# Optimization experiments

Measured on AMD Instinct MI355X. Metric: run time of the kernel, lower is better.

Reference implementation:

```python
import jax, jax.numpy as jnp
import numpy as np

B, L, D = 4, 896, 2048
HQ, HKV, HD = 32, 8, 64
GROUP = HQ // HKV          # 4
TOKENS_PER_FRAME = 7
ROPE_BASE = 10000.0


def setup_inputs() -> dict:
    key = jax.random.key(0)
    ks = jax.random.split(key, 5)
    s = 0.02
    return {
        "x": jax.random.normal(ks[0], (B, L, D), jnp.float32),
        "wq": jax.random.normal(ks[1], (D, D), jnp.float32) * s,
        "wk": jax.random.normal(ks[2], (D, HKV * HD), jnp.float32) * s,
        "wv": jax.random.normal(ks[3], (D, HKV * HD), jnp.float32) * s,
        "wo": jax.random.normal(ks[4], (D, D), jnp.float32) * s,
        "pos_ids": jnp.arange(L, dtype=jnp.int32),
    }


def _apply_rotary(t, cos, sin):
    # t: [B, L, H, HD]; rotate all HD dims, interleaved pairs.
    Bt, Lt, Ht, Hd = t.shape
    tp = t.reshape(Bt, Lt, Ht, Hd // 2, 2)
    x1, x2 = tp[..., 0], tp[..., 1]
    c = cos[None, :, None, :]   # [1, L, 1, HD/2]
    s = sin[None, :, None, :]
    y1 = x1 * c - x2 * s
    y2 = x1 * s + x2 * c
    return jnp.stack([y1, y2], axis=-1).reshape(Bt, Lt, Ht, Hd)


def reference(x, wq, wk, wv, wo, pos_ids):
    Bx, Lx, Dx = x.shape
    q = (x @ wq).reshape(Bx, Lx, HQ, HD)
    k = (x @ wk).reshape(Bx, Lx, HKV, HD)
    v = (x @ wv).reshape(Bx, Lx, HKV, HD)

    # RoPE (rot_dim = head_dim), scale = 1.0
    half = HD // 2
    inv_freq = 1.0 / (ROPE_BASE ** (jnp.arange(half, dtype=jnp.float32) / half))
    freqs = pos_ids.astype(jnp.float32)[:, None] * inv_freq[None, :]  # [L, HD/2]
    cos, sin = jnp.cos(freqs), jnp.sin(freqs)
    q = _apply_rotary(q, cos, sin)
    k = _apply_rotary(k, cos, sin)

    # GQA: expand kv heads to q heads (kv_head = q_head // GROUP)
    k = jnp.repeat(k, GROUP, axis=2)   # [B, L, HQ, HD]
    v = jnp.repeat(v, GROUP, axis=2)

    scale = 1.0 / jnp.sqrt(jnp.float32(HD))
    scores = jnp.einsum('blhd,bmhd->bhlm', q, k) * scale  # [B, HQ, L, L]

    # frame-block causal mask: allow key frame <= query frame
    pos = jnp.arange(Lx)
    fid = pos // TOKENS_PER_FRAME
    allow = fid[None, :] <= fid[:, None]                  # [L, L]
    neg = jnp.finfo(scores.dtype).min
    scores = jnp.where(allow[None, None], scores, neg)

    probs = jax.nn.softmax(scores, axis=-1)
    out = jnp.einsum('bhlm,bmhd->blhd', probs, v).reshape(Bx, Lx, Dx)
    return out @ wo
```

## Files before the change

kernel.cpp:

```cpp
#include <hip/hip_runtime.h>
#include <hip/hip_bf16.h>
#include <cstdint>

typedef __bf16 bf16;
typedef __bf16 bf16x8 __attribute__((ext_vector_type(8)));
typedef float floatx4 __attribute__((ext_vector_type(4)));

#define B_   4
#define L_   896
#define D_   2048
#define HQ_  32
#define HKV_ 8
#define HD_  64
#define NQKV 3072
#define M_   3584

__device__ inline void gl_lds16(const bf16* g, bf16* l) {
    __builtin_amdgcn_global_load_lds(
        (const __attribute__((address_space(1))) void*)g,
        (__attribute__((address_space(3))) void*)l, 16, 0, 0);
}

__device__ inline void barrier_() {
    asm volatile("" ::: "memory");
    __builtin_amdgcn_s_barrier();
    asm volatile("" ::: "memory");
}

__global__ __launch_bounds__(256) void convert_to_bf16(const float* __restrict__ in,
                                                       bf16* __restrict__ out) {
    long q = (long)blockIdx.x * 256 + threadIdx.x;
    float4 v = ((const float4*)in)[q];
    union { bf16 b[4]; ushort4 u; } w;
    w.b[0] = (bf16)v.x; w.b[1] = (bf16)v.y; w.b[2] = (bf16)v.z; w.b[3] = (bf16)v.w;
    ((ushort4*)out)[q] = w.u;
}

__global__ __launch_bounds__(256) void rope_cs_kernel(const int* __restrict__ pos_ids,
                                                      float2* __restrict__ cs) {
    int idx = blockIdx.x * 256 + threadIdx.x;
    if (idx >= L_ * 32) return;
    int l = idx >> 5, i = idx & 31;
    float p = (float)pos_ids[l];
    float inv = exp2f(-(float)i * (13.287712379549449f / 32.0f));
    float a = p * inv;
    cs[idx] = make_float2(cosf(a), sinf(a));
}

__global__ __launch_bounds__(256) void transpose_cvt(
    const float* __restrict__ in, ushort* __restrict__ out, int C, int R) {
    __shared__ ushort t[64][72];
    int tid = threadIdx.x;
    int tr = tid >> 4, tc = (tid & 15) << 2;
    long r0 = (long)blockIdx.y << 6, c0 = (long)blockIdx.x << 6;
#pragma unroll
    for (int i = 0; i < 4; ++i) {
        float4 v = *(const float4*)&in[(r0 + tr + i * 16) * C + c0 + tc];
        union { bf16 b[4]; ushort4 u; } w;
        w.b[0] = (bf16)v.x; w.b[1] = (bf16)v.y; w.b[2] = (bf16)v.z; w.b[3] = (bf16)v.w;
        *(ushort4*)&t[tr + i * 16][tc] = w.u;
    }
    __syncthreads();
#pragma unroll
    for (int i = 0; i < 4; ++i) {
        ushort4 w;
        w.x = t[tc + 0][tr + i * 16];
        w.y = t[tc + 1][tr + i * 16];
        w.z = t[tc + 2][tr + i * 16];
        w.w = t[tc + 3][tr + i * 16];
        *(ushort4*)&out[(c0 + tr + i * 16) * R + r0 + tc] = w;
    }
}

__global__ __launch_bounds__(256) void transpose_u16(
    const ushort* __restrict__ in, ushort* __restrict__ out,
    int ld_in, int ld_out, long is1, long is2, long os1, long os2) {
    __shared__ ushort t[64][72];
    int z = blockIdx.z;
    const ushort* ip = in + (long)(z >> 3) * is1 + (long)(z & 7) * is2;
    ushort* op = out + (long)(z >> 3) * os1 + (long)(z & 7) * os2;
    int tid = threadIdx.x;
    int tr = tid >> 4, tc = (tid & 15) << 2;
    long r0 = (long)blockIdx.y << 6, c0 = (long)blockIdx.x << 6;
#pragma unroll
    for (int i = 0; i < 4; ++i) {
        ushort4 v = *(const ushort4*)&ip[(r0 + tr + i * 16) * ld_in + c0 + tc];
        *(ushort4*)&t[tr + i * 16][tc] = v;
    }
    __syncthreads();
#pragma unroll
    for (int i = 0; i < 4; ++i) {
        ushort4 w;
        w.x = t[tc + 0][tr + i * 16];
        w.y = t[tc + 1][tr + i * 16];
        w.z = t[tc + 2][tr + i * 16];
        w.w = t[tc + 3][tr + i * 16];
        *(ushort4*)&op[(c0 + tr + i * 16) * ld_out + r0 + tc] = w;
    }
}


template <int RQ, int RESPAN>
__device__ inline void lda_g(const bf16* p, int l16, int c0, int c1, bf16x8 (&af)[4][2]) {
#pragma unroll
    for (int i = 0; i < 4; ++i) {
        const bf16* rp = &p[(RQ * RESPAN + i * 16 + l16) * 64];
        af[i][0] = *(const bf16x8*)&rp[c0];
        af[i][1] = *(const bf16x8*)&rp[c1];
    }
}

template <int CQ>
__device__ inline void ldb_g(const bf16* p, int brow, int l16, int c0, int c1,
                             bf16x8 (&bq)[2][2]) {
#pragma unroll
    for (int j = 0; j < 2; ++j) {
        const bf16* rp = &p[(brow + (CQ * 2 + j) * 16 + l16) * 64];
        bq[j][0] = *(const bf16x8*)&rp[c0];
        bq[j][1] = *(const bf16x8*)&rp[c1];
    }
}

__device__ inline void stage_half(const bf16* gsrc, bf16* ldst, long rowK) {
    gl_lds16(gsrc,            ldst);
    gl_lds16(gsrc + 8 * rowK, ldst + 512);
}

template <int RQ, int CQ>
__device__ inline void mma8(const bf16x8 (&af)[4][2], const bf16x8 (&bq)[2][2],
                            floatx4 (&acc)[8][4]) {
#pragma unroll
    for (int i = 0; i < 4; ++i)
#pragma unroll
        for (int j = 0; j < 2; ++j) {
            floatx4 c = acc[RQ * 4 + i][CQ * 2 + j];
            c = __builtin_amdgcn_mfma_f32_16x16x32_bf16(af[i][0], bq[j][0], c, 0, 0, 0);
            c = __builtin_amdgcn_mfma_f32_16x16x32_bf16(af[i][1], bq[j][1], c, 0, 0, 0);
            acc[RQ * 4 + i][CQ * 2 + j] = c;
        }
}

__global__ __launch_bounds__(512, 2) void gemm256(
    const bf16* __restrict__ A, const bf16* __restrict__ Bt, void* __restrict__ C,
    int Ntot, int Ktot, int outf32, int ropeflag, const float2* __restrict__ cs) {
    __shared__ bf16 lds[2][2][2][128 * 64];
    const int tid = threadIdx.x;
    const int w = tid >> 6, lane = tid & 63;
    const int quad = lane >> 4, l16 = lane & 15;
    const int wr = w >> 2, wc = w & 3;

    const int gx = gridDim.x;
    const int nwg = gx * gridDim.y;
    int orig = blockIdx.y * gx + blockIdx.x;
    int q8 = nwg >> 3, r8 = nwg & 7;
    int xcd = orig & 7, lid = orig >> 3;
    int wg = (xcd < r8 ? xcd * (q8 + 1) : r8 * (q8 + 1) + (xcd - r8) * q8) + lid;
    const long m0 = (long)(wg / gx) << 8;
    const long n0 = (long)(wg % gx) << 8;

    const long rowK = Ktot;
    const int srow = w * 16 + (lane >> 3);
    const int scol = ((lane & 7) ^ (lane >> 3)) << 3;
    const bf16* baseA = A  + (m0 + srow) * rowK + scol;
    const bf16* baseB = Bt + (n0 + srow) * rowK + scol;
    const int d0 = w * 1024 + lane * 8;

    const int m7 = l16 & 7;
    const int col0 = ((0 + quad) ^ m7) << 3;
    const int col1 = ((4 + quad) ^ m7) << 3;
    const int brow = (wc & 1) * 64;

    floatx4 acc[8][4];
#pragma unroll
    for (int i = 0; i < 8; ++i)
#pragma unroll
        for (int j = 0; j < 4; ++j)
#pragma unroll
            for (int r = 0; r < 4; ++r) acc[i][j][r] = 0.f;

    bf16x8 af[4][2], bq0[2][2], bq1[2][2];

    const int T = Ktot >> 6;
    stage_half(baseA,                   &lds[0][0][0][d0], rowK);
    stage_half(baseA + 128 * rowK,      &lds[0][0][1][d0], rowK);
    stage_half(baseB,                   &lds[0][1][0][d0], rowK);
    stage_half(baseB + 128 * rowK,      &lds[0][1][1][d0], rowK);
    stage_half(baseB + 64,              &lds[1][1][0][d0], rowK);
    stage_half(baseB + 128 * rowK + 64, &lds[1][1][1][d0], rowK);
    asm volatile("s_waitcnt vmcnt(4)" ::: "memory");
    barrier_();

    for (int t = 0; t < T; ++t) {
        const int cur = t & 1, nxt = cur ^ 1;
        const bf16* pa = &lds[cur][0][wr][0];
        const bf16* pb = &lds[cur][1][wc >> 1][0];
        const long koff  = (long)(t + 1) * 64;
        const long koff2 = (long)(t + 2) * 64;

        lda_g<0, 64>(pa, l16, col0, col1, af);
        ldb_g<0>(pb, brow, l16, col0, col1, bq0);
        if (t + 1 < T) stage_half(baseA + koff, &lds[nxt][0][0][d0], rowK);
        barrier_();
        asm volatile("s_waitcnt lgkmcnt(0)" ::: "memory");
        __builtin_amdgcn_sched_barrier(0);
        __builtin_amdgcn_s_setprio(1);
        mma8<0, 0>(af, bq0, acc);
        __builtin_amdgcn_s_setprio(0);
        barrier_();

        ldb_g<1>(pb, brow, l16, col0, col1, bq1);
        if (t + 1 < T) stage_half(baseA + 128 * rowK + koff, &lds[nxt][0][1][d0], rowK);
        barrier_();
        asm volatile("s_waitcnt lgkmcnt(0)" ::: "memory");
        __builtin_amdgcn_sched_barrier(0);
        __builtin_amdgcn_s_setprio(1);
        mma8<0, 1>(af, bq1, acc);
        __builtin_amdgcn_s_setprio(0);
        barrier_();

        lda_g<1, 64>(pa, l16, col0, col1, af);
        if (t + 2 < T) stage_half(baseB + koff2, &lds[cur][1][0][d0], rowK);
        barrier_();
        asm volatile("s_waitcnt lgkmcnt(0)" ::: "memory");
        __builtin_amdgcn_sched_barrier(0);
        __builtin_amdgcn_s_setprio(1);
        mma8<1, 0>(af, bq0, acc);
        __builtin_amdgcn_s_setprio(0);
        barrier_();

        if (t + 2 < T) stage_half(baseB + 128 * rowK + koff2, &lds[cur][1][1][d0], rowK);
        barrier_();
        asm volatile("s_waitcnt lgkmcnt(0)" ::: "memory");
        __builtin_amdgcn_sched_barrier(0);
        __builtin_amdgcn_s_setprio(1);
        mma8<1, 1>(af, bq1, acc);
        __builtin_amdgcn_s_setprio(0);
        if (t + 2 < T) asm volatile("s_waitcnt vmcnt(4)" ::: "memory");
        else           asm volatile("s_waitcnt vmcnt(0)" ::: "memory");
        barrier_();
    }

    const int dorope = ropeflag && (n0 < 2560);
    const float sgn = (lane & 1) ? 1.f : -1.f;
#pragma unroll
    for (int ri = 0; ri < 8; ++ri)
#pragma unroll
        for (int j = 0; j < 4; ++j)
#pragma unroll
            for (int r = 0; r < 4; ++r) {
                long m = m0 + wr * 128 + ri * 16 + quad * 4 + r;
                long n = n0 + wc * 64 + j * 16 + l16;
                float v = acc[ri][j][r];
                if (dorope) {
                    int l = (int)(m % L_);
                    float2 csv = cs[l * 32 + ((int)(n >> 1) & 31)];
                    float p = __shfl_xor(v, 1);
                    v = v * csv.x + p * sgn * csv.y;
                }
                if (outf32) ((float*)C)[m * Ntot + n] = v;
                else        ((bf16*)C)[m * Ntot + n] = (bf16)v;
            }
}

template <int CH>
__device__ inline void mma4(const bf16x8 (&af)[4][2], const bf16x8 (&bq)[2][2],
                            floatx4 (&acc)[4][4]) {
#pragma unroll
    for (int i = 0; i < 4; ++i)
#pragma unroll
        for (int j = 0; j < 2; ++j) {
            floatx4 c = acc[i][CH * 2 + j];
            c = __builtin_amdgcn_mfma_f32_16x16x32_bf16(af[i][0], bq[j][0], c, 0, 0, 0);
            c = __builtin_amdgcn_mfma_f32_16x16x32_bf16(af[i][1], bq[j][1], c, 0, 0, 0);
            acc[i][CH * 2 + j] = c;
        }
}

__global__ __launch_bounds__(512, 2) void gemm256x128(
    const bf16* __restrict__ A, const bf16* __restrict__ Bt, float* __restrict__ C,
    int Ntot, int Ktot) {
    __shared__ bf16 ldsA[2][2][128 * 64];
    __shared__ bf16 ldsB[3][128 * 64];
    const int tid = threadIdx.x;
    const int w = tid >> 6, lane = tid & 63;
    const int quad = lane >> 4, l16 = lane & 15;
    const int wr = w >> 1, wc = w & 1;

    const int gx = gridDim.x;
    const int nwg = gx * gridDim.y;
    int orig = blockIdx.y * gx + blockIdx.x;
    int q8 = nwg >> 3, r8 = nwg & 7;
    int xcd = orig & 7, lid = orig >> 3;
    int wg = (xcd < r8 ? xcd * (q8 + 1) : r8 * (q8 + 1) + (xcd - r8) * q8) + lid;
    const long m0 = (long)(wg / gx) << 8;
    const long n0 = (long)(wg % gx) << 7;

    const long rowK = Ktot;
    const int srow = w * 16 + (lane >> 3);
    const int scol = ((lane & 7) ^ (lane >> 3)) << 3;
    const bf16* baseA = A  + (m0 + srow) * rowK + scol;
    const bf16* baseB = Bt + (n0 + srow) * rowK + scol;
    const int d0 = w * 1024 + lane * 8;

    const int m7 = l16 & 7;
    const int col0 = ((0 + quad) ^ m7) << 3;
    const int col1 = ((4 + quad) ^ m7) << 3;
    const int arow = (wr & 1) * 64;
    const int brow = wc * 64;

    floatx4 acc[4][4];
#pragma unroll
    for (int i = 0; i < 4; ++i)
#pragma unroll
        for (int j = 0; j < 4; ++j)
#pragma unroll
            for (int r = 0; r < 4; ++r) acc[i][j][r] = 0.f;

    bf16x8 af[4][2], bq0[2][2], bq1[2][2];

    const int T = Ktot >> 6;
    stage_half(baseA,              &ldsA[0][0][d0], rowK);
    stage_half(baseA + 128 * rowK, &ldsA[0][1][d0], rowK);
    stage_half(baseB,              &ldsB[0][d0],    rowK);
    stage_half(baseB + 64,         &ldsB[1][d0],    rowK);
    asm volatile("s_waitcnt vmcnt(2)" ::: "memory");
    barrier_();

    int bs = 0;
    for (int t = 0; t < T; ++t) {
        const int cur = t & 1, nxt = cur ^ 1;
        const bf16* pa = &ldsA[cur][wr >> 1][0];
        const bf16* pb = &ldsB[bs][0];
        const long koff  = (long)(t + 1) * 64;
        const long koff2 = (long)(t + 2) * 64;
        const int bs2 = bs >= 1 ? bs - 1 : 2;

        lda_g<0, 0>(pa, arow + l16, col0, col1, af);
        ldb_g<0>(pb, brow, l16, col0, col1, bq0);
        if (t + 1 < T) {
            stage_half(baseA + koff,              &ldsA[nxt][0][d0], rowK);
            stage_half(baseA + 128 * rowK + koff, &ldsA[nxt][1][d0], rowK);
        }
        barrier_();
        asm volatile("s_waitcnt lgkmcnt(0)" ::: "memory");
        __builtin_amdgcn_sched_barrier(0);
        __builtin_amdgcn_s_setprio(1);
        mma4<0>(af, bq0, acc);
        __builtin_amdgcn_s_setprio(0);
        barrier_();

        ldb_g<1>(pb, brow, l16, col0, col1, bq1);
        if (t + 2 < T) stage_half(baseB + koff2, &ldsB[bs2][d0], rowK);
        barrier_();
        asm volatile("s_waitcnt lgkmcnt(0)" ::: "memory");
        __builtin_amdgcn_sched_barrier(0);
        __builtin_amdgcn_s_setprio(1);
        mma4<1>(af, bq1, acc);
        __builtin_amdgcn_s_setprio(0);
        if      (t + 2 < T) asm volatile("s_waitcnt vmcnt(2)" ::: "memory");
        else if (t + 1 < T) asm volatile("s_waitcnt vmcnt(0)" ::: "memory");
        barrier_();
        bs = bs < 2 ? bs + 1 : 0;
    }

#pragma unroll
    for (int i = 0; i < 4; ++i)
#pragma unroll
        for (int j = 0; j < 4; ++j)
#pragma unroll
            for (int r = 0; r < 4; ++r) {
                long m = m0 + wr * 64 + i * 16 + quad * 4 + r;
                long n = n0 + wc * 64 + j * 16 + l16;
                C[m * Ntot + n] = acc[i][j][r];
            }
}

__global__ __launch_bounds__(256) void attn_kernel(
    const bf16* __restrict__ QKV,
    const bf16* __restrict__ Vt,
    bf16* __restrict__ AO) {
    __shared__ bf16 Ks[64 * 72];
    __shared__ bf16 Vs[64 * 72];
    __shared__ bf16 Ps[4][16 * 72];
    const int tid  = threadIdx.x;
    const int wid  = tid >> 6, lane = tid & 63;
    const int quad = lane >> 4, c = lane & 15;
    const int b = blockIdx.z, hq = blockIdx.y, kvh = hq >> 2;
    const int q0b = blockIdx.x * 64;
    const int q0 = q0b + wid * 16;
    bf16* ps = &Ps[wid][0];

    const bf16* Qb = QKV + ((long)(b * L_ + q0)) * NQKV + hq * HD_;
    const bf16* Kb = QKV + ((long)(b * L_)) * NQKV + D_ + kvh * HD_;
    const bf16* Vb = Vt + ((long)(b * HKV_ + kvh)) * (HD_ * L_);

    bf16x8 qf0 = *(const bf16x8*)&Qb[(long)c * NQKV + quad * 8];
    bf16x8 qf1 = *(const bf16x8*)&Qb[(long)c * NQKV + 32 + quad * 8];

    float lsum[4];
    floatx4 o[4];
#pragma unroll
    for (int r = 0; r < 4; r++) lsum[r] = 0.f;
#pragma unroll
    for (int nt = 0; nt < 4; nt++)
#pragma unroll
        for (int r = 0; r < 4; r++) o[nt][r] = 0.f;

    int fe[4];
#pragma unroll
    for (int r = 0; r < 4; r++) { int l = q0 + quad * 4 + r; fe[r] = (l / 7 + 1) * 7; }
    const int kend = ((q0b + 63) / 7 + 1) * 7;

    const int srow = tid >> 3, schunk = (tid & 7) << 3;

    for (int k0 = 0; k0 < kend; k0 += 64) {
        bf16x8 kg0 = *(const bf16x8*)&Kb[(long)(k0 + srow) * NQKV + schunk];
        bf16x8 kg1 = *(const bf16x8*)&Kb[(long)(k0 + 32 + srow) * NQKV + schunk];
        bf16x8 vg0 = *(const bf16x8*)&Vb[(long)srow * L_ + k0 + schunk];
        bf16x8 vg1 = *(const bf16x8*)&Vb[(long)(srow + 32) * L_ + k0 + schunk];
        __syncthreads();
        *(bf16x8*)&Ks[srow * 72 + schunk]        = kg0;
        *(bf16x8*)&Ks[(srow + 32) * 72 + schunk] = kg1;
        *(bf16x8*)&Vs[srow * 72 + schunk]        = vg0;
        *(bf16x8*)&Vs[(srow + 32) * 72 + schunk] = vg1;
        __syncthreads();

        floatx4 s[4];
#pragma unroll
        for (int n = 0; n < 4; n++) {
#pragma unroll
            for (int r = 0; r < 4; r++) s[n][r] = 0.f;
            bf16x8 kf0 = *(bf16x8*)&Ks[(n * 16 + c) * 72 + quad * 8];
            bf16x8 kf1 = *(bf16x8*)&Ks[(n * 16 + c) * 72 + 32 + quad * 8];
            s[n] = __builtin_amdgcn_mfma_f32_16x16x32_bf16(qf0, kf0, s[n], 0, 0, 0);
            s[n] = __builtin_amdgcn_mfma_f32_16x16x32_bf16(qf1, kf1, s[n], 0, 0, 0);
        }
#pragma unroll
        for (int n = 0; n < 4; n++) {
            const int key = k0 + n * 16 + c;
#pragma unroll
            for (int r = 0; r < 4; r++) {
                float e = __expf(fmaf(s[n][r], 0.125f, -12.0f));
                e = (key < fe[r]) ? e : 0.f;
                lsum[r] += e;
                ps[(quad * 4 + r) * 72 + n * 16 + c] = (bf16)e;
            }
        }
        bf16x8 pf0 = *(bf16x8*)&ps[c * 72 + quad * 8];
        bf16x8 pf1 = *(bf16x8*)&ps[c * 72 + 32 + quad * 8];
#pragma unroll
        for (int nt = 0; nt < 4; nt++) {
            bf16x8 vf0 = *(bf16x8*)&Vs[(nt * 16 + c) * 72 + quad * 8];
            bf16x8 vf1 = *(bf16x8*)&Vs[(nt * 16 + c) * 72 + 32 + quad * 8];
            o[nt] = __builtin_amdgcn_mfma_f32_16x16x32_bf16(pf0, vf0, o[nt], 0, 0, 0);
            o[nt] = __builtin_amdgcn_mfma_f32_16x16x32_bf16(pf1, vf1, o[nt], 0, 0, 0);
        }
    }
#pragma unroll
    for (int r = 0; r < 4; r++) {
#pragma unroll
        for (int off = 1; off < 16; off <<= 1) lsum[r] += __shfl_xor(lsum[r], off);
    }
#pragma unroll
    for (int nt = 0; nt < 4; nt++)
#pragma unroll
        for (int r = 0; r < 4; r++) {
            int l = q0 + quad * 4 + r;
            AO[((long)(b * L_ + l)) * D_ + hq * HD_ + nt * 16 + c] = (bf16)(o[nt][r] / lsum[r]);
        }
}

extern "C" void kernel_launch(void* const* d_in, const int* in_sizes, int n_in,
                              void* d_out, int out_size, void* d_ws, size_t ws_size,
                              hipStream_t stream) {
    (void)in_sizes; (void)n_in; (void)out_size; (void)ws_size;
    const float* x  = (const float*)d_in[0];
    const float* wq = (const float*)d_in[1];
    const float* wk = (const float*)d_in[2];
    const float* wv = (const float*)d_in[3];
    const float* wo = (const float*)d_in[4];
    const int* pos  = (const int*)d_in[5];

    bf16* ws    = (bf16*)d_ws;
    bf16* xb    = ws;
    bf16* wqkvT = ws + 7340032L;
    bf16* woT   = ws + 13631488L;
    bf16* QKV   = ws + 17825792L;
    bf16* Vt    = ws + 28835840L;
    bf16* AO    = xb;
    float2* cs  = (float2*)(ws + 30670848L);

    convert_to_bf16<<<dim3(7168), 256, 0, stream>>>(x, xb);
    rope_cs_kernel<<<dim3(112), dim3(256), 0, stream>>>(pos, cs);

    transpose_cvt<<<dim3(32, 32), 256, 0, stream>>>(wq, (ushort*)wqkvT, 2048, 2048);
    transpose_cvt<<<dim3(8, 32), 256, 0, stream>>>(wk, (ushort*)(wqkvT + 4194304L), 512, 2048);
    transpose_cvt<<<dim3(8, 32), 256, 0, stream>>>(wv, (ushort*)(wqkvT + 5242880L), 512, 2048);
    transpose_cvt<<<dim3(32, 32), 256, 0, stream>>>(wo, (ushort*)woT, 2048, 2048);

    gemm256<<<dim3(12, 14), 512, 0, stream>>>(xb, wqkvT, QKV, NQKV, D_, 0, 1, cs);

    transpose_u16<<<dim3(1, 14, 32), 256, 0, stream>>>(
        (const ushort*)(QKV + 2560), (ushort*)Vt, 3072, 896,
        896L * 3072, 64, 8L * 57344, 57344);

    attn_kernel<<<dim3(14, 32, 4), 256, 0, stream>>>(QKV, Vt, AO);

    gemm256x128<<<dim3(16, 14), 512, 0, stream>>>(AO, woT, (float*)d_out, D_, D_);
}
```

Baseline: 306.9 us.

## Share K/V tiles across GQA group in attention; move RoPE to separate kernel

The attention kernel now assigns one block per KV head, and each of its four waves handles one query head of the group over 64 query rows. Each K/V tile loaded into LDS is therefore reused by four query heads instead of one, which cuts global K/V traffic and the block count by a factor of four. In exchange each wave does more work and needs more registers, and the grid drops to 448 blocks. RoPE is taken out of the QKV GEMM epilogue and done by a separate vectorized pass over the QKV buffer, adding one launch and an extra read/write of Q and K.

```diff
diff --git a/kernel.cpp b/kernel.cpp
--- a/kernel.cpp
+++ b/kernel.cpp
@@ -45,6 +45,26 @@
     float inv = exp2f(-(float)i * (13.287712379549449f / 32.0f));
     float a = p * inv;
     cs[idx] = make_float2(cosf(a), sinf(a));
+}
+
+__global__ __launch_bounds__(256) void rope_apply(bf16* __restrict__ QKV,
+                                                  const float2* __restrict__ cs) {
+    int idx = blockIdx.x * 256 + threadIdx.x;
+    int m = idx / 320, g = idx - m * 320;
+    int l = m % L_;
+    int hp = (g * 4) & 31;
+    const float2* ct = &cs[l * 32 + hp];
+    bf16* p = QKV + (long)m * NQKV + g * 8;
+    bf16x8 v = *(bf16x8*)p;
+    bf16x8 w;
+#pragma unroll
+    for (int i = 0; i < 4; i++) {
+        float2 csv = ct[i];
+        float x1 = (float)v[2 * i], x2 = (float)v[2 * i + 1];
+        w[2 * i]     = (bf16)(x1 * csv.x - x2 * csv.y);
+        w[2 * i + 1] = (bf16)(x1 * csv.y + x2 * csv.x);
+    }
+    *(bf16x8*)p = w;
 }
 
 __global__ __launch_bounds__(256) void transpose_cvt(
@@ -142,7 +162,7 @@
 
 __global__ __launch_bounds__(512, 2) void gemm256(
     const bf16* __restrict__ A, const bf16* __restrict__ Bt, void* __restrict__ C,
-    int Ntot, int Ktot, int outf32, int ropeflag, const float2* __restrict__ cs) {
+    int Ntot, int Ktot, int outf32) {
     __shared__ bf16 lds[2][2][2][128 * 64];
     const int tid = threadIdx.x;
     const int w = tid >> 6, lane = tid & 63;
@@ -240,8 +260,6 @@
         barrier_();
     }
 
-    const int dorope = ropeflag && (n0 < 2560);
-    const float sgn = (lane & 1) ? 1.f : -1.f;
 #pragma unroll
     for (int ri = 0; ri < 8; ++ri)
 #pragma unroll
@@ -250,15 +268,8 @@
             for (int r = 0; r < 4; ++r) {
                 long m = m0 + wr * 128 + ri * 16 + quad * 4 + r;
                 long n = n0 + wc * 64 + j * 16 + l16;
-                float v = acc[ri][j][r];
-                if (dorope) {
-                    int l = (int)(m % L_);
-                    float2 csv = cs[l * 32 + ((int)(n >> 1) & 31)];
-                    float p = __shfl_xor(v, 1);
-                    v = v * csv.x + p * sgn * csv.y;
-                }
-                if (outf32) ((float*)C)[m * Ntot + n] = v;
-                else        ((bf16*)C)[m * Ntot + n] = (bf16)v;
+                if (outf32) ((float*)C)[m * Ntot + n] = acc[ri][j][r];
+                else        ((bf16*)C)[m * Ntot + n] = (bf16)acc[ri][j][r];
             }
 }
 
@@ -381,34 +392,47 @@
     bf16* __restrict__ AO) {
     __shared__ bf16 Ks[64 * 72];
     __shared__ bf16 Vs[64 * 72];
-    __shared__ bf16 Ps[4][16 * 72];
+    __shared__ bf16 Ps[4][64 * 72];
     const int tid  = threadIdx.x;
     const int wid  = tid >> 6, lane = tid & 63;
     const int quad = lane >> 4, c = lane & 15;
-    const int b = blockIdx.z, hq = blockIdx.y, kvh = hq >> 2;
+    const int b = blockIdx.z, kvh = blockIdx.y;
+    const int hq = kvh * 4 + wid;
     const int q0b = blockIdx.x * 64;
-    const int q0 = q0b + wid * 16;
     bf16* ps = &Ps[wid][0];
 
-    const bf16* Qb = QKV + ((long)(b * L_ + q0)) * NQKV + hq * HD_;
+    const bf16* Qb = QKV + ((long)(b * L_ + q0b)) * NQKV + hq * HD_;
     const bf16* Kb = QKV + ((long)(b * L_)) * NQKV + D_ + kvh * HD_;
     const bf16* Vb = Vt + ((long)(b * HKV_ + kvh)) * (HD_ * L_);
 
-    bf16x8 qf0 = *(const bf16x8*)&Qb[(long)c * NQKV + quad * 8];
-    bf16x8 qf1 = *(const bf16x8*)&Qb[(long)c * NQKV + 32 + quad * 8];
-
-    float lsum[4];
-    floatx4 o[4];
-#pragma unroll
-    for (int r = 0; r < 4; r++) lsum[r] = 0.f;
-#pragma unroll
-    for (int nt = 0; nt < 4; nt++)
-#pragma unroll
-        for (int r = 0; r < 4; r++) o[nt][r] = 0.f;
-
-    int fe[4];
-#pragma unroll
-    for (int r = 0; r < 4; r++) { int l = q0 + quad * 4 + r; fe[r] = (l / 7 + 1) * 7; }
+    bf16x8 qf[4][2];
+#pragma unroll
+    for (int a = 0; a < 4; a++) {
+        qf[a][0] = *(const bf16x8*)&Qb[(long)(a * 16 + c) * NQKV + quad * 8];
+        qf[a][1] = *(const bf16x8*)&Qb[(long)(a * 16 + c) * NQKV + 32 + quad * 8];
+    }
+
+    float lsum[4][4];
+    floatx4 o[4][4];
+#pragma unroll
+    for (int a = 0; a < 4; a++)
+#pragma unroll
+        for (int r = 0; r < 4; r++) lsum[a][r] = 0.f;
+#pragma unroll
+    for (int a = 0; a < 4; a++)
+#pragma unroll
+        for (int nt = 0; nt < 4; nt++)
+#pragma unroll
+            for (int r = 0; r < 4; r++) o[a][nt][r] = 0.f;
+
+    int fe[4][4];
+#pragma unroll
+    for (int a = 0; a < 4; a++)
+#pragma unroll
+        for (int r = 0; r < 4; r++) {
+            int l = q0b + a * 16 + quad * 4 + r;
+            fe[a][r] = (l / 7 + 1) * 7;
+        }
     const int kend = ((q0b + 63) / 7 + 1) * 7;
 
     const int srow = tid >> 3, schunk = (tid & 7) << 3;
@@ -425,49 +449,68 @@
         *(bf16x8*)&Vs[(srow + 32) * 72 + schunk] = vg1;
         __syncthreads();
 
-        floatx4 s[4];
+        bf16x8 kf[4][2];
 #pragma unroll
         for (int n = 0; n < 4; n++) {
-#pragma unroll
-            for (int r = 0; r < 4; r++) s[n][r] = 0.f;
-            bf16x8 kf0 = *(bf16x8*)&Ks[(n * 16 + c) * 72 + quad * 8];
-            bf16x8 kf1 = *(bf16x8*)&Ks[(n * 16 + c) * 72 + 32 + quad * 8];
-            s[n] = __builtin_amdgcn_mfma_f32_16x16x32_bf16(qf0, kf0, s[n], 0, 0, 0);
-            s[n] = __builtin_amdgcn_mfma_f32_16x16x32_bf16(qf1, kf1, s[n], 0, 0, 0);
-        }
-#pragma unroll
-        for (int n = 0; n < 4; n++) {
-            const int key = k0 + n * 16 + c;
+            kf[n][0] = *(bf16x8*)&Ks[(n * 16 + c) * 72 + quad * 8];
+            kf[n][1] = *(bf16x8*)&Ks[(n * 16 + c) * 72 + 32 + quad * 8];
+        }
+#pragma unroll
+        for (int a = 0; a < 4; a++) {
+            floatx4 s[4];
+#pragma unroll
+            for (int n = 0; n < 4; n++) {
+#pragma unroll
+                for (int r = 0; r < 4; r++) s[n][r] = 0.f;
+                s[n] = __builtin_amdgcn_mfma_f32_16x16x32_bf16(qf[a][0], kf[n][0], s[n], 0, 0, 0);
+                s[n] = __builtin_amdgcn_mfma_f32_16x16x32_bf16(qf[a][1], kf[n][1], s[n], 0, 0, 0);
+            }
+#pragma unroll
+            for (int n = 0; n < 4; n++) {
+                const int key = k0 + n * 16 + c;
+#pragma unroll
+                for (int r = 0; r < 4; r++) {
+                    float e = __expf(fmaf(s[n][r], 0.125f, -12.0f));
+                    e = (key < fe[a][r]) ? e : 0.f;
+                    lsum[a][r] += e;
+                    ps[(a * 16 + quad * 4 + r) * 72 + n * 16 + c] = (bf16)e;
+                }
+            }
+        }
+        bf16x8 vf[4][2];
+#pragma unroll
+        for (int nt = 0; nt < 4; nt++) {
+            vf[nt][0] = *(bf16x8*)&Vs[(nt * 16 + c) * 72 + quad * 8];
+            vf[nt][1] = *(bf16x8*)&Vs[(nt * 16 + c) * 72 + 32 + quad * 8];
+        }
+#pragma unroll
+        for (int a = 0; a < 4; a++) {
+            bf16x8 pf0 = *(bf16x8*)&ps[(a * 16 + c) * 72 + quad * 8];
+            bf16x8 pf1 = *(bf16x8*)&ps[(a * 16 + c) * 72 + 32 + quad * 8];
+#pragma unroll
+            for (int nt = 0; nt < 4; nt++) {
+                o[a][nt] = __builtin_amdgcn_mfma_f32_16x16x32_bf16(pf0, vf[nt][0], o[a][nt], 0, 0, 0);
+                o[a][nt] = __builtin_amdgcn_mfma_f32_16x16x32_bf16(pf1, vf[nt][1], o[a][nt], 0, 0, 0);
+            }
+        }
+    }
+#pragma unroll
+    for (int a = 0; a < 4; a++)
+#pragma unroll
+        for (int r = 0; r < 4; r++) {
+#pragma unroll
+            for (int off = 1; off < 16; off <<= 1) lsum[a][r] += __shfl_xor(lsum[a][r], off);
+        }
+#pragma unroll
+    for (int a = 0; a < 4; a++)
+#pragma unroll
+        for (int nt = 0; nt < 4; nt++)
 #pragma unroll
             for (int r = 0; r < 4; r++) {
-                float e = __expf(fmaf(s[n][r], 0.125f, -12.0f));
-                e = (key < fe[r]) ? e : 0.f;
-                lsum[r] += e;
-                ps[(quad * 4 + r) * 72 + n * 16 + c] = (bf16)e;
+                int l = q0b + a * 16 + quad * 4 + r;
+                AO[((long)(b * L_ + l)) * D_ + hq * HD_ + nt * 16 + c] =
+                    (bf16)(o[a][nt][r] / lsum[a][r]);
             }
-        }
-        bf16x8 pf0 = *(bf16x8*)&ps[c * 72 + quad * 8];
-        bf16x8 pf1 = *(bf16x8*)&ps[c * 72 + 32 + quad * 8];
-#pragma unroll
-        for (int nt = 0; nt < 4; nt++) {
-            bf16x8 vf0 = *(bf16x8*)&Vs[(nt * 16 + c) * 72 + quad * 8];
-            bf16x8 vf1 = *(bf16x8*)&Vs[(nt * 16 + c) * 72 + 32 + quad * 8];
-            o[nt] = __builtin_amdgcn_mfma_f32_16x16x32_bf16(pf0, vf0, o[nt], 0, 0, 0);
-            o[nt] = __builtin_amdgcn_mfma_f32_16x16x32_bf16(pf1, vf1, o[nt], 0, 0, 0);
-        }
-    }
-#pragma unroll
-    for (int r = 0; r < 4; r++) {
-#pragma unroll
-        for (int off = 1; off < 16; off <<= 1) lsum[r] += __shfl_xor(lsum[r], off);
-    }
-#pragma unroll
-    for (int nt = 0; nt < 4; nt++)
-#pragma unroll
-        for (int r = 0; r < 4; r++) {
-            int l = q0 + quad * 4 + r;
-            AO[((long)(b * L_ + l)) * D_ + hq * HD_ + nt * 16 + c] = (bf16)(o[nt][r] / lsum[r]);
-        }
 }
 
 extern "C" void kernel_launch(void* const* d_in, const int* in_sizes, int n_in,
@@ -498,13 +541,15 @@
     transpose_cvt<<<dim3(8, 32), 256, 0, stream>>>(wv, (ushort*)(wqkvT + 5242880L), 512, 2048);
     transpose_cvt<<<dim3(32, 32), 256, 0, stream>>>(wo, (ushort*)woT, 2048, 2048);
 
-    gemm256<<<dim3(12, 14), 512, 0, stream>>>(xb, wqkvT, QKV, NQKV, D_, 0, 1, cs);
+    gemm256<<<dim3(12, 14), 512, 0, stream>>>(xb, wqkvT, QKV, NQKV, D_, 0);
+
+    rope_apply<<<dim3(4480), 256, 0, stream>>>(QKV, cs);
 
     transpose_u16<<<dim3(1, 14, 32), 256, 0, stream>>>(
         (const ushort*)(QKV + 2560), (ushort*)Vt, 3072, 896,
         896L * 3072, 64, 8L * 57344, 57344);
 
-    attn_kernel<<<dim3(14, 32, 4), 256, 0, stream>>>(QKV, Vt, AO);
+    attn_kernel<<<dim3(14, 8, 4), 256, 0, stream>>>(QKV, Vt, AO);
 
     gemm256x128<<<dim3(16, 14), 512, 0, stream>>>(AO, woT, (float*)d_out, D_, D_);
 }
```

New measurement: 285.9 us. -6.8%, faster.
